# Kernel tuning notes

Hardware: AMD Instinct MI355X
Metric: run time of the kernel (lower is better)

## Reference

```python
import jax, jax.numpy as jnp
import numpy as np

B, S, T = 1024, 1024, 32  # batch, seq_len, num_tags


def setup_inputs() -> dict:
    key = jax.random.key(0)
    k1, k2, k3, k4 = jax.random.split(key, 4)
    logits = jax.random.normal(k1, (B, S, T), dtype=jnp.float32)
    transitions = jax.random.normal(k2, (T, T), dtype=jnp.float32)
    tags = jax.random.randint(k3, (B, S), 0, T)
    lengths = jax.random.randint(k4, (B,), 1, S + 1)
    return {"logits": logits, "transitions": transitions, "tags": tags, "lengths": lengths}


def _forward_alg(logits, transitions):
    # viterbi_0 = logits[:, 0, :]; then for t>=1:
    # v_next[b, j] = logsumexp_i(v[b, i] + trans[i, j]) + logits[b, t, j]
    v0 = logits[:, 0, :]  # (B, T)
    emits = jnp.swapaxes(logits[:, 1:, :], 0, 1)  # (S-1, B, T)

    def step(v, emit_t):
        v_next = jax.nn.logsumexp(v[:, :, None] + transitions[None, :, :], axis=1) + emit_t
        return v_next, None

    v_final, _ = jax.lax.scan(step, v0, emits)
    return jax.nn.logsumexp(v_final, axis=1)  # (B,)


def _score_sentence(logits, transitions, tags, lengths):
    # emission scores of gold tags, masked to t < length (note: original ignores
    # lengths in the forward algorithm but uses them here, faithfully reproduced)
    emit = jnp.take_along_axis(logits, tags[:, :, None], axis=2)[..., 0]  # (B, S)
    pos = jnp.arange(S)
    emit_mask = (pos[None, :] < lengths[:, None]).astype(logits.dtype)
    score = jnp.sum(emit * emit_mask, axis=1)
    # transition scores trans[tags[t-1], tags[t]] for 1 <= t < length
    trans_sc = transitions[tags[:, :-1], tags[:, 1:]]  # (B, S-1)
    trans_mask = (pos[None, 1:] < lengths[:, None]).astype(logits.dtype)
    score = score + jnp.sum(trans_sc * trans_mask, axis=1)
    return score  # (B,)


def reference(logits, transitions, tags, lengths):
    log_z = _forward_alg(logits, transitions)
    gold = _score_sentence(logits, transitions, tags, lengths)
    return jnp.mean(log_z - gold)
```

## Files before the change

### kernel.cpp

```cpp
#include <hip/hip_runtime.h>

#define NB 1024
#define NS 1024
#define NT 32
#define L2E 1.44269504088896340736f
#define LN2 0.69314718055994530942f

typedef short        bfrag  __attribute__((ext_vector_type(8)));
typedef float        cfrag  __attribute__((ext_vector_type(16)));
typedef __bf16       bf16x2 __attribute__((ext_vector_type(2)));
typedef float        f32x8  __attribute__((ext_vector_type(8)));
typedef float        f32x2  __attribute__((ext_vector_type(2)));
typedef unsigned int u32;
typedef unsigned int u32x2v __attribute__((ext_vector_type(2)));
typedef unsigned int u32x4  __attribute__((ext_vector_type(4)));

__device__ __forceinline__ float fexp2(float x){ return __builtin_amdgcn_exp2f(x); }
__device__ __forceinline__ float flog2(float x){ return __builtin_amdgcn_logf(x); }

__device__ __forceinline__ u32 pkbf(float a, float b){
    f32x2 t; t.x = a; t.y = b;
    return __builtin_bit_cast(u32, __builtin_convertvector(t, bf16x2));
}
__device__ __forceinline__ bfrag mk_afrag(f32x8 v){
    u32x4 r;
    r[0] = pkbf(v[0], v[1]); r[1] = pkbf(v[2], v[3]);
    r[2] = pkbf(v[4], v[5]); r[3] = pkbf(v[6], v[7]);
    return __builtin_bit_cast(bfrag, r);
}

#if __has_builtin(__builtin_amdgcn_permlane32_swap)
#define HAVE_PLSWAP 1
#else
#define HAVE_PLSWAP 0
#endif

__device__ __forceinline__ void half_swap(u32 &x, u32 &y, int h){
#if HAVE_PLSWAP
    u32x2v r = __builtin_amdgcn_permlane32_swap(x, y, false, false);
    x = r[0]; y = r[1];
#else
    u32 X  = __shfl_xor(h ? x : y, 32, 64);
    u32 nx = h ? X : x;
    u32 ny = h ? y : X;
    x = nx; y = ny;
#endif
}

template<int N> struct ic { static constexpr int value = N; };
union accu { cfrag c; f32x2 p[8]; };

__global__ __launch_bounds__(256, 8) void crf_chunk(
    const float* __restrict__ logits, const float* __restrict__ trans,
    u32* __restrict__ wmat, float* __restrict__ woff)
{
    __shared__ __align__(16) float dscall[4 * 512];

    const int tid = threadIdx.x;
    const int wv  = tid >> 6, lt = tid & 63;
    const int m   = lt & 31,  h  = lt >> 5;
    const int bc  = blockIdx.x * 4 + wv;
    const int b   = bc >> 3,  c  = bc & 7;
    float* dsc = dscall + wv * 512;

    const float* base = logits + (size_t)b * NS * NT;

    f32x8 Et0, Et1;
    #pragma unroll
    for (int j = 0; j < 8; j++){
        Et0[j] = fexp2(L2E * trans[(     8*h + j)*NT + m]);
        Et1[j] = fexp2(L2E * trans[(16 + 8*h + j)*NT + m]);
    }
    const bfrag A0f = mk_afrag(Et0);
    const bfrag A1f = mk_afrag(Et1);

    u32x4 B0v, B1v;
    #pragma unroll
    for (int d = 0; d < 4; d++){
        int k0 = 8*h + 2*d;      u32 v = 0;
        if (k0     == m) v |= 0x3F80u;
        if (k0 + 1 == m) v |= 0x3F800000u;
        B0v[d] = v;
        int k1 = 16 + 8*h + 2*d; v = 0;
        if (k1     == m) v |= 0x3F80u;
        if (k1 + 1 == m) v |= 0x3F800000u;
        B1v[d] = v;
    }

    cfrag zacc;
    #pragma unroll
    for (int q = 0; q < 16; q++) zacc[q] = 0.0f;

    float off = 0.0f;
    const int tbeg = c*128 + 1;

    float eA[4], eB[4];

    auto issue = [&](float (&e)[4], int k){
        const int t0 = tbeg + k*8 + 4*h;
        #pragma unroll
        for (int i = 0; i < 4; i++){
            int t = t0 + i; t = t > (NS-1) ? (NS-1) : t;
            e[i] = base[t*NT + m];
        }
    };
    auto commit = [&](float (&e)[4], int k){
        float* sp = dsc + (k & 1)*256 + (4*h)*32 + m;
        #pragma unroll
        for (int i = 0; i < 4; i++) sp[i*32] = fexp2(L2E * e[i]);
    };

    auto procN = [&](int k, auto nstc){
        constexpr int NST = decltype(nstc)::value;
        const float* db = dsc + (k & 1)*256 + 4*h;
        #pragma unroll
        for (int i = 0; i < NST; i++){
            accu acc;
            acc.c = __builtin_amdgcn_mfma_f32_32x32x16_bf16(
                        A0f, __builtin_bit_cast(bfrag, B0v), zacc, 0, 0, 0);
            acc.c = __builtin_amdgcn_mfma_f32_32x32x16_bf16(
                        A1f, __builtin_bit_cast(bfrag, B1v), acc.c, 0, 0, 0);

            const f32x2* d0 = (const f32x2*)(db + i*32 +  0);
            const f32x2* d1 = (const f32x2*)(db + i*32 +  8);
            const f32x2* d2 = (const f32x2*)(db + i*32 + 16);
            const f32x2* d3 = (const f32x2*)(db + i*32 + 24);
            acc.p[0] *= d0[0]; acc.p[1] *= d0[1];
            acc.p[2] *= d1[0]; acc.p[3] *= d1[1];
            acc.p[4] *= d2[0]; acc.p[5] *= d2[1];
            acc.p[6] *= d3[0]; acc.p[7] *= d3[1];

            if (i == 7){
                float x  = acc.c[0];
                float xo = __shfl_xor(x, 32, 64);
                float xs = h ? xo : x;
                u32 xb = __builtin_bit_cast(u32, xs);
                int ex = (int)((xb >> 23) & 0xFFu);
                ex = ex < 24 ? 24 : (ex > 230 ? 230 : ex);
                off += (float)(ex - 127);
                f32x2 s2;
                s2.x = s2.y = __builtin_bit_cast(float, (u32)(254 - ex) << 23);
                #pragma unroll
                for (int q = 0; q < 8; q++) acc.p[q] *= s2;
            }

            u32 P0 = pkbf(acc.c[0],  acc.c[1]),  P1 = pkbf(acc.c[2],  acc.c[3]);
            u32 P2 = pkbf(acc.c[4],  acc.c[5]),  P3 = pkbf(acc.c[6],  acc.c[7]);
            u32 P4 = pkbf(acc.c[8],  acc.c[9]),  P5 = pkbf(acc.c[10], acc.c[11]);
            u32 P6 = pkbf(acc.c[12], acc.c[13]), P7 = pkbf(acc.c[14], acc.c[15]);
            half_swap(P0, P2, h); half_swap(P1, P3, h);
            half_swap(P4, P6, h); half_swap(P5, P7, h);
            B0v[0]=P0; B0v[1]=P1; B0v[2]=P2; B0v[3]=P3;
            B1v[0]=P4; B1v[1]=P5; B1v[2]=P6; B1v[3]=P7;
        }
    };

    issue(eA, 0); commit(eA, 0);
    #pragma unroll 1
    for (int k = 0; k < 14; k += 2){
        issue(eB, k + 1);
        procN(k, ic<8>{});
        commit(eB, k + 1);
        issue(eA, k + 2);
        procN(k + 1, ic<8>{});
        commit(eA, k + 2);
    }
    issue(eB, 15);
    procN(14, ic<8>{});
    commit(eB, 15);
    if (c != 7) procN(15, ic<8>{});
    else        procN(15, ic<7>{});

    const size_t mb = (size_t)bc * 512;
    #pragma unroll
    for (int d = 0; d < 4; d++){
        wmat[mb + d*64 + lt]     = B0v[d];
        wmat[mb + (4+d)*64 + lt] = B1v[d];
    }
    if (h == 0) woff[bc*32 + m] = off;
}

__global__ __launch_bounds__(64) void crf_combine(
    const float* __restrict__ logits, const float* __restrict__ trans,
    const int* __restrict__ tags, const int* __restrict__ lens,
    const u32* __restrict__ wmat, const float* __restrict__ woff,
    float* __restrict__ out)
{
    __shared__ __align__(16) float ldsT[NT*NT];
    __shared__ __align__(16) int   ldsTag[NS];
    __shared__ __align__(16) float ldsU[NT];

    const int tid = threadIdx.x;
    const int m   = tid & 31;
    const int b   = blockIdx.x;
    const int len = lens[b];
    const float* lgb = logits + (size_t)b * NS * NT;

    #pragma unroll
    for (int i = 0; i < 16; i++) ldsT[tid + i*64] = trans[tid + i*64];
    const int4* tg4 = (const int4*)(tags + b*NS);
    #pragma unroll
    for (int i = 0; i < 4; i++) ((int4*)ldsTag)[tid + i*64] = tg4[tid + i*64];
    __syncthreads();

    float g = 0.0f;
    #pragma unroll
    for (int it = 0; it < 16; it++){
        int t = tid + it*64;
        if (t < len){
            int tg = ldsTag[t];
            g += lgb[t*NT + tg];
            if (t >= 1) g += ldsT[ldsTag[t-1]*NT + tg];
        }
    }

    float v = fexp2(L2E * lgb[m]);
    float voff = 0.0f;

    const int n  = m;
    const int f  = n >> 4;
    const int hh = (n >> 3) & 1;
    const int di = f*4 + ((n >> 1) & 3);

    for (int cc = 0; cc < 8; cc++){
        const int bcn = b*8 + cc;
        float offm = woff[bcn*32 + m];
        float w = flog2(v) + offm;
        float mw = w;
        #pragma unroll
        for (int d = 1; d <= 16; d <<= 1) mw = fmaxf(mw, __shfl_xor(mw, d, 64));
        float u = fexp2(w - mw);
        if (tid < 32) ldsU[m] = u;
        __syncthreads();

        const uint4* mp = (const uint4*)(wmat + (size_t)bcn*512 + di*64 + hh*32);
        float acc = 0.0f;
        #pragma unroll
        for (int qq = 0; qq < 8; qq++){
            uint4  md = mp[qq];
            float4 uu = ((const float4*)ldsU)[qq];
            float e0 = __builtin_bit_cast(float, (n&1) ? (md.x & 0xFFFF0000u) : (md.x << 16));
            float e1 = __builtin_bit_cast(float, (n&1) ? (md.y & 0xFFFF0000u) : (md.y << 16));
            float e2 = __builtin_bit_cast(float, (n&1) ? (md.z & 0xFFFF0000u) : (md.z << 16));
            float e3 = __builtin_bit_cast(float, (n&1) ? (md.w & 0xFFFF0000u) : (md.w << 16));
            acc = fmaf(e0, uu.x, acc);
            acc = fmaf(e1, uu.y, acc);
            acc = fmaf(e2, uu.z, acc);
            acc = fmaf(e3, uu.w, acc);
        }
        v = acc;
        voff += mw;
        __syncthreads();
    }

    float s = v;
    #pragma unroll
    for (int d = 1; d <= 16; d <<= 1) s += __shfl_xor(s, d, 64);
    #pragma unroll
    for (int d = 1; d <= 32; d <<= 1) g += __shfl_xor(g, d, 64);
    if (tid == 0){
        float logz = LN2 * (voff + flog2(s));
        atomicAdd(out, (logz - g) * (1.0f / (float)NB));
    }
}

extern "C" void kernel_launch(void* const* d_in, const int* in_sizes, int n_in,
                              void* d_out, int out_size, void* d_ws, size_t ws_size,
                              hipStream_t stream) {
    const float* logits = (const float*)d_in[0];
    const float* trans  = (const float*)d_in[1];
    const int*   tags   = (const int*)d_in[2];
    const int*   lens   = (const int*)d_in[3];

    u32*   wmat = (u32*)d_ws;
    float* woff = (float*)(wmat + 8192*512);

    hipMemsetAsync(d_out, 0, sizeof(float), stream);
    crf_chunk  <<<2048, 256, 0, stream>>>(logits, trans, wmat, woff);
    crf_combine<<<1024, 64, 0, stream>>>(logits, trans, tags, lens, wmat, woff,
                                         (float*)d_out);
}
```

Baseline: 266.9 us.

## Streamline chunk recurrence: truncating bf16 pack, uniform rescale, deferred exponent folding

```diff
diff --git a/kernel.cpp b/kernel.cpp
--- a/kernel.cpp
+++ b/kernel.cpp
@@ -10,6 +10,7 @@
 typedef float        cfrag  __attribute__((ext_vector_type(16)));
 typedef __bf16       bf16x2 __attribute__((ext_vector_type(2)));
 typedef float        f32x8  __attribute__((ext_vector_type(8)));
+typedef float        f32x4  __attribute__((ext_vector_type(4)));
 typedef float        f32x2  __attribute__((ext_vector_type(2)));
 typedef unsigned int u32;
 typedef unsigned int u32x2v __attribute__((ext_vector_type(2)));
@@ -18,14 +19,18 @@
 __device__ __forceinline__ float fexp2(float x){ return __builtin_amdgcn_exp2f(x); }
 __device__ __forceinline__ float flog2(float x){ return __builtin_amdgcn_logf(x); }
 
-__device__ __forceinline__ u32 pkbf(float a, float b){
+__device__ __forceinline__ u32 pkbf_rne(float a, float b){
     f32x2 t; t.x = a; t.y = b;
     return __builtin_bit_cast(u32, __builtin_convertvector(t, bf16x2));
 }
+__device__ __forceinline__ u32 pkbf_t(float a, float b){
+    return __builtin_amdgcn_perm(__builtin_bit_cast(u32, b),
+                                 __builtin_bit_cast(u32, a), 0x07060302u);
+}
 __device__ __forceinline__ bfrag mk_afrag(f32x8 v){
     u32x4 r;
-    r[0] = pkbf(v[0], v[1]); r[1] = pkbf(v[2], v[3]);
-    r[2] = pkbf(v[4], v[5]); r[3] = pkbf(v[6], v[7]);
+    r[0] = pkbf_rne(v[0], v[1]); r[1] = pkbf_rne(v[2], v[3]);
+    r[2] = pkbf_rne(v[4], v[5]); r[3] = pkbf_rne(v[6], v[7]);
     return __builtin_bit_cast(bfrag, r);
 }
 
@@ -49,6 +54,7 @@
 
 template<int N> struct ic { static constexpr int value = N; };
 union accu { cfrag c; f32x2 p[8]; };
+union q4u  { f32x4 v; f32x2 p[2]; };
 
 __global__ __launch_bounds__(256, 8) void crf_chunk(
     const float* __restrict__ logits, const float* __restrict__ trans,
@@ -91,7 +97,8 @@
     #pragma unroll
     for (int q = 0; q < 16; q++) zacc[q] = 0.0f;
 
-    float off = 0.0f;
+    int   offi = 0;
+    float exf  = 0.0f;
     const int tbeg = c*128 + 1;
 
     float eA[4], eB[4];
@@ -106,11 +113,21 @@
     };
     auto commit = [&](float (&e)[4], int k){
         float* sp = dsc + (k & 1)*256 + (4*h)*32 + m;
-        #pragma unroll
-        for (int i = 0; i < 4; i++) sp[i*32] = fexp2(L2E * e[i]);
+        float a0 = (h == 0) ? -exf : 0.0f;
+        sp[0]    = fexp2(fmaf(L2E, e[0], a0));
+        sp[32]   = fexp2(L2E * e[1]);
+        sp[64]   = fexp2(L2E * e[2]);
+        sp[96]   = fexp2(L2E * e[3]);
     };
 
-    auto procN = [&](int k, auto nstc){
+    auto exref = [&](float ref)->int{
+        u32 xb = __builtin_bit_cast(u32, ref);
+        u32 xf = __builtin_amdgcn_readfirstlane(xb);
+        int ex = (int)((xf >> 23) & 0xFFu) - 127;
+        return ex < -120 ? -120 : (ex > 120 ? 120 : ex);
+    };
+
+    auto procN = [&](int k, bool defer, auto nstc){
         constexpr int NST = decltype(nstc)::value;
         const float* db = dsc + (k & 1)*256 + 4*h;
         #pragma unroll
@@ -121,33 +138,34 @@
             acc.c = __builtin_amdgcn_mfma_f32_32x32x16_bf16(
                         A1f, __builtin_bit_cast(bfrag, B1v), acc.c, 0, 0, 0);
 
-            const f32x2* d0 = (const f32x2*)(db + i*32 +  0);
-            const f32x2* d1 = (const f32x2*)(db + i*32 +  8);
-            const f32x2* d2 = (const f32x2*)(db + i*32 + 16);
-            const f32x2* d3 = (const f32x2*)(db + i*32 + 24);
-            acc.p[0] *= d0[0]; acc.p[1] *= d0[1];
-            acc.p[2] *= d1[0]; acc.p[3] *= d1[1];
-            acc.p[4] *= d2[0]; acc.p[5] *= d2[1];
-            acc.p[6] *= d3[0]; acc.p[7] *= d3[1];
-
-            if (i == 7){
-                float x  = acc.c[0];
-                float xo = __shfl_xor(x, 32, 64);
-                float xs = h ? xo : x;
-                u32 xb = __builtin_bit_cast(u32, xs);
-                int ex = (int)((xb >> 23) & 0xFFu);
-                ex = ex < 24 ? 24 : (ex > 230 ? 230 : ex);
-                off += (float)(ex - 127);
+            q4u d0, d1, d2, d3;
+            d0.v = *(const f32x4*)(db + i*32 +  0);
+            d1.v = *(const f32x4*)(db + i*32 +  8);
+            d2.v = *(const f32x4*)(db + i*32 + 16);
+            d3.v = *(const f32x4*)(db + i*32 + 24);
+            acc.p[0] *= d0.p[0]; acc.p[1] *= d0.p[1];
+            acc.p[2] *= d1.p[0]; acc.p[3] *= d1.p[1];
+            acc.p[4] *= d2.p[0]; acc.p[5] *= d2.p[1];
+            acc.p[6] *= d3.p[0]; acc.p[7] *= d3.p[1];
+
+            if (i == 3){
+                int ex = exref(fmaxf(acc.c[0], acc.c[8]));
+                offi += ex;
                 f32x2 s2;
-                s2.x = s2.y = __builtin_bit_cast(float, (u32)(254 - ex) << 23);
+                s2.x = s2.y = __builtin_bit_cast(float, (u32)(127 - ex) << 23);
                 #pragma unroll
                 for (int q = 0; q < 8; q++) acc.p[q] *= s2;
             }
-
-            u32 P0 = pkbf(acc.c[0],  acc.c[1]),  P1 = pkbf(acc.c[2],  acc.c[3]);
-            u32 P2 = pkbf(acc.c[4],  acc.c[5]),  P3 = pkbf(acc.c[6],  acc.c[7]);
-            u32 P4 = pkbf(acc.c[8],  acc.c[9]),  P5 = pkbf(acc.c[10], acc.c[11]);
-            u32 P6 = pkbf(acc.c[12], acc.c[13]), P7 = pkbf(acc.c[14], acc.c[15]);
+            if (i == 7 && defer){
+                int ex = exref(fmaxf(acc.c[0], acc.c[8]));
+                offi += ex;
+                exf = (float)ex;
+            }
+
+            u32 P0 = pkbf_t(acc.c[0],  acc.c[1]),  P1 = pkbf_t(acc.c[2],  acc.c[3]);
+            u32 P2 = pkbf_t(acc.c[4],  acc.c[5]),  P3 = pkbf_t(acc.c[6],  acc.c[7]);
+            u32 P4 = pkbf_t(acc.c[8],  acc.c[9]),  P5 = pkbf_t(acc.c[10], acc.c[11]);
+            u32 P6 = pkbf_t(acc.c[12], acc.c[13]), P7 = pkbf_t(acc.c[14], acc.c[15]);
             half_swap(P0, P2, h); half_swap(P1, P3, h);
             half_swap(P4, P6, h); half_swap(P5, P7, h);
             B0v[0]=P0; B0v[1]=P1; B0v[2]=P2; B0v[3]=P3;
@@ -159,17 +177,17 @@
     #pragma unroll 1
     for (int k = 0; k < 14; k += 2){
         issue(eB, k + 1);
-        procN(k, ic<8>{});
+        procN(k, true, ic<8>{});
         commit(eB, k + 1);
         issue(eA, k + 2);
-        procN(k + 1, ic<8>{});
+        procN(k + 1, true, ic<8>{});
         commit(eA, k + 2);
     }
     issue(eB, 15);
-    procN(14, ic<8>{});
+    procN(14, true, ic<8>{});
     commit(eB, 15);
-    if (c != 7) procN(15, ic<8>{});
-    else        procN(15, ic<7>{});
+    if (c != 7) procN(15, false, ic<8>{});
+    else        procN(15, false, ic<7>{});
 
     const size_t mb = (size_t)bc * 512;
     #pragma unroll
@@ -177,7 +195,7 @@
         wmat[mb + d*64 + lt]     = B0v[d];
         wmat[mb + (4+d)*64 + lt] = B1v[d];
     }
-    if (h == 0) woff[bc*32 + m] = off;
+    if (lt == 0) woff[bc] = (float)offi;
 }
 
 __global__ __launch_bounds__(64) void crf_combine(
@@ -224,8 +242,8 @@
 
     for (int cc = 0; cc < 8; cc++){
         const int bcn = b*8 + cc;
-        float offm = woff[bcn*32 + m];
-        float w = flog2(v) + offm;
+        float offc = woff[bcn];
+        float w = flog2(v) + offc;
         float mw = w;
         #pragma unroll
         for (int d = 1; d <= 16; d <<= 1) mw = fmaxf(mw, __shfl_xor(mw, d, 64));
```

Measured after the change: 263.7 us. About the same (-1.2%).
